# Kernel tuning notes

Hardware: AMD Instinct MI355X
Metric: run time of the kernel (lower is better)

Reference implementation:

```python
import jax, jax.numpy as jnp
import numpy as np

B, N, F_IN = 32, 512, 64
HEADS = (8, 8)
HIDS = (64, 64)
EDGE_P = 0.05  # graph density
NEG_SLOPE = 0.2
NEG_INF = -1e20


def setup_inputs() -> dict:
    key = jax.random.key(0)
    ks = jax.random.split(key, 8)
    x = jax.random.normal(ks[0], (B, N, F_IN), dtype=jnp.float32)
    adj = (jax.random.uniform(ks[1], (B, N, N)) < EDGE_P).astype(jnp.float32)
    adj = jnp.maximum(adj, adj.transpose(0, 2, 1))  # symmetric adjacency
    # mask = (batch, row): every (b, n) pair gets the masked softmax
    b_idx = jnp.repeat(jnp.arange(B, dtype=jnp.int32), N)   # [B*N]
    r_idx = jnp.tile(jnp.arange(N, dtype=jnp.int32), B)     # [B*N]
    # layer 0: f_in=64 -> f_out=64, H=8 ; layer 1: f_in=64*8=512 -> f_out=64, H=8
    W0 = jax.random.normal(ks[2], (F_IN, HIDS[0]), dtype=jnp.float32) / jnp.sqrt(jnp.float32(F_IN))
    a_src0 = jax.random.normal(ks[3], (HIDS[0], HEADS[0]), dtype=jnp.float32) / jnp.sqrt(jnp.float32(HIDS[0]))
    a_dst0 = jax.random.normal(ks[4], (HIDS[0], HEADS[0]), dtype=jnp.float32) / jnp.sqrt(jnp.float32(HIDS[0]))
    f_in1 = HIDS[0] * HEADS[0]
    W1 = jax.random.normal(ks[5], (f_in1, HIDS[1]), dtype=jnp.float32) / jnp.sqrt(jnp.float32(f_in1))
    a_src1 = jax.random.normal(ks[6], (HIDS[1], HEADS[1]), dtype=jnp.float32) / jnp.sqrt(jnp.float32(HIDS[1]))
    a_dst1 = jax.random.normal(ks[7], (HIDS[1], HEADS[1]), dtype=jnp.float32) / jnp.sqrt(jnp.float32(HIDS[1]))
    return dict(x=x, adj=adj, b_idx=b_idx, r_idx=r_idx,
                W0=W0, a_src0=a_src0, a_dst0=a_dst0,
                W1=W1, a_src1=a_src1, a_dst1=a_dst1)


def _gat_layer(x, adj, b_idx, r_idx, W, a_src, a_dst):
    # x: [B,N,f_in], adj: [B,N,N] (diag already set), W: [f_in,F], a_*: [F,H]
    hp = x @ W                                        # [B,N,F]
    s = jnp.einsum('bnf,fh->bhn', hp, a_src)          # attn_src
    d = jnp.einsum('bnf,fh->bhn', hp, a_dst)          # attn_dst
    attn = s[:, :, :, None] + d[:, :, None, :]        # [B,H,N,N]
    attn = jnp.where(attn >= 0, attn, NEG_SLOPE * attn)  # leaky_relu(0.2)
    attn = jnp.where(adj[:, None, :, :] == 0, 0.0, attn)  # masked_fill(adj==0, 0)
    rows = attn[b_idx, :, r_idx, :]                   # [K,H,N]
    rows = jnp.where(rows == 0.0, NEG_INF, rows)
    rows = jax.nn.softmax(rows, axis=-1)
    attn = attn.at[b_idx, :, r_idx, :].set(rows)
    return jnp.einsum('bhij,bjf->bhif', attn, hp)     # [B,H,N,F]


def reference(x, adj, b_idx, r_idx, W0, a_src0, a_dst0, W1, a_src1, a_dst1):
    Bn, Nn = x.shape[:2]
    # torch mutates adj in place: adj[batch,row,row] = 1 (self loops)
    adj = adj.at[b_idx, r_idx, r_idx].set(1.0)
    o = _gat_layer(x, adj, b_idx, r_idx, W0, a_src0, a_dst0)      # [B,H,N,F0]
    x1 = jax.nn.elu(o.transpose(0, 2, 1, 3).reshape(Bn, Nn, -1))  # [B,N,H*F0]
    o2 = _gat_layer(x1, adj, b_idx, r_idx, W1, a_src1, a_dst1)    # [B,H,N,F1]
    return o2.mean(axis=1)                                        # [B,N,F1]
```

## Files before the change

kernel.cpp:

```cpp
#include <hip/hip_runtime.h>
#include <hip/hip_bf16.h>
#include <math.h>

#define BB 32
#define NN 512

typedef _Float16 f16x8 __attribute__((ext_vector_type(8)));
typedef __fp16  fp16x2 __attribute__((ext_vector_type(2)));
typedef float f32x4 __attribute__((ext_vector_type(4)));

#define MFMA16(a, b, c) __builtin_amdgcn_mfma_f32_16x16x32_f16(a, b, c, 0, 0, 0)

union AF { f16x8 v; unsigned int u[4]; };

__device__ __forceinline__ void gload_lds16(const void* g, void* l) {
    __builtin_amdgcn_global_load_lds(
        (const __attribute__((address_space(1))) unsigned int*)g,
        (__attribute__((address_space(3))) unsigned int*)l, 16, 0, 0);
}

__global__ __launch_bounds__(256) void k_wt_prep(
    const float* __restrict__ W0, _Float16* __restrict__ W0T,
    const float* __restrict__ W1, _Float16* __restrict__ W1T)
{
    int id = blockIdx.x * 256 + threadIdx.x;
    const float* W; _Float16* WT; int KT, task;
    if (id < 512) { W = W0; WT = W0T; KT = 64;  task = id; }
    else          { W = W1; WT = W1T; KT = 512; task = id - 512; }
    int n = task & 63, gabs = task >> 6;
    int c = gabs >> 3, g = gabs & 7;
    f16x8 hv;
#pragma unroll
    for (int e = 0; e < 8; ++e)
        hv[e] = (_Float16)W[(size_t)(gabs * 8 + e) * 64 + n];
    *(f16x8*)(WT + (size_t)n * KT + c * 64 + (g ^ (n & 7)) * 8) = hv;
}

__global__ __launch_bounds__(256) void k_maxd(
    const float* __restrict__ dTg, float* __restrict__ maxd)
{
    __shared__ float sm[4];
    int bh = blockIdx.x;
    int t = threadIdx.x, lane = t & 63, w = t >> 6;
    const float* p = dTg + (size_t)bh * NN;
    float m = fmaxf(p[t], p[t + 256]);
#pragma unroll
    for (int off = 32; off; off >>= 1) m = fmaxf(m, __shfl_xor(m, off));
    if (lane == 0) sm[w] = m;
    __syncthreads();
    if (t == 0) maxd[bh] = fmaxf(fmaxf(sm[0], sm[1]), fmaxf(sm[2], sm[3]));
}

static __device__ __forceinline__ void epi_sd_hpt(
    const float* ctile, const float* asd_f, int row0, int t,
    float* __restrict__ s, float* __restrict__ dTg, _Float16* __restrict__ hpT)
{
    int b = row0 >> 9, jb = row0 & 511;
    if (t < 128) {
        int rr = t >> 3, h = t & 7;
        float sv = 0.f, dv = 0.f;
#pragma unroll
        for (int f = 0; f < 64; ++f) {
            float hv = ctile[rr * 66 + f];
            sv = fmaf(hv, asd_f[f * 8 + h], sv);
            dv = fmaf(hv, asd_f[512 + f * 8 + h], dv);
        }
        s[((size_t)b * NN + jb + rr) * 8 + h] = sv;
        dTg[((size_t)b * 8 + h) * NN + jb + rr] = dv;
    } else {
        int t2 = t - 128;
        int f = t2 >> 1, jl = (t2 & 1) * 8;
        f16x8 hv;
#pragma unroll
        for (int e = 0; e < 8; ++e)
            hv[e] = (_Float16)ctile[(jl + e) * 66 + f];
        *(f16x8*)(hpT + ((size_t)b * 64 + f) * NN + jb + jl) = hv;
    }
}

__global__ __launch_bounds__(256) void k_gemm0(
    const float* __restrict__ x, const _Float16* __restrict__ W0T,
    const float* __restrict__ a_src, const float* __restrict__ a_dst,
    const float* __restrict__ adj, unsigned long long* __restrict__ adjb,
    float* __restrict__ s, float* __restrict__ dTg, _Float16* __restrict__ hpT)
{
    __shared__ float ctile[16 * 66];
    __shared__ float asd_f[1024];
    __shared__ unsigned int mrow[16][16];
    int t = threadIdx.x, row0 = blockIdx.x * 16;
    int lane = t & 63, w = t >> 6, cn = lane & 15, rq = lane >> 4;

    int ar = t >> 4, seg = t & 15;
    const float* ap = adj + (size_t)(row0 + ar) * NN + seg * 32;
    float4 av[8];
#pragma unroll
    for (int q = 0; q < 8; ++q) av[q] = ((const float4*)ap)[q];

    ((float4*)asd_f)[t] = (t < 128) ? ((const float4*)a_src)[t]
                                    : ((const float4*)a_dst)[t - 128];
    f32x4 acc;
#pragma unroll
    for (int e = 0; e < 4; ++e) acc[e] = 0.f;
#pragma unroll
    for (int ks = 0; ks < 2; ++ks) {
        const float* xp = x + (size_t)(row0 + cn) * 64 + ks * 32 + rq * 8;
        float4 x0 = *(const float4*)xp, x1 = *(const float4*)(xp + 4);
        f16x8 ah = {(_Float16)x0.x, (_Float16)x0.y, (_Float16)x0.z, (_Float16)x0.w,
                    (_Float16)x1.x, (_Float16)x1.y, (_Float16)x1.z, (_Float16)x1.w};
        int nn = w * 16 + cn;
        f16x8 bh = *(const f16x8*)(W0T + (size_t)nn * 64 + (((ks * 4 + rq) ^ (nn & 7)) * 8));
        acc = MFMA16(ah, bh, acc);
    }
#pragma unroll
    for (int r = 0; r < 4; ++r)
        ctile[(rq * 4 + r) * 66 + w * 16 + cn] = acc[r];
    __syncthreads();
    epi_sd_hpt(ctile, asd_f, row0, t, s, dTg, hpT);

    unsigned int m32 = 0;
#pragma unroll
    for (int q = 0; q < 8; ++q) {
        if (av[q].x != 0.f) m32 |= 1u << (q * 4 + 0);
        if (av[q].y != 0.f) m32 |= 1u << (q * 4 + 1);
        if (av[q].z != 0.f) m32 |= 1u << (q * 4 + 2);
        if (av[q].w != 0.f) m32 |= 1u << (q * 4 + 3);
    }
    int i = (row0 + ar) & (NN - 1);
    if ((i >> 5) == seg) m32 |= 1u << (i & 31);
    mrow[ar][seg] = m32;
    __syncthreads();
    if (t < 128) {
        int r = t >> 3, k = t & 7;
        unsigned long long u = (unsigned long long)mrow[r][2 * k]
                             | ((unsigned long long)mrow[r][2 * k + 1] << 32);
        adjb[(size_t)(row0 + r) * 8 + k] = u;
    }
}

#define LD8(DST0, DST1, J)                                              \
    do {                                                                \
        *(float4*)&DST0[0] = *(const float4*)(dg0 + (J));               \
        *(float4*)&DST0[4] = *(const float4*)(dg0 + (J) + 4);           \
        *(float4*)&DST1[0] = *(const float4*)(dg1 + (J));               \
        *(float4*)&DST1[4] = *(const float4*)(dg1 + (J) + 4);           \
    } while (0)

#define PSTEP(DD0v, DD1v, MBYTE, KS, HTC)                               \
    do {                                                                \
        AF aA, aB;                                                      \
        _Pragma("unroll")                                               \
        for (int e = 0; e < 8; e += 2) {                                \
            float pA[2], pB[2];                                         \
            _Pragma("unroll")                                           \
            for (int q = 0; q < 2; ++q) {                               \
                int ee = e + q;                                         \
                bool con = (MBYTE >> ee) & 1u;                          \
                float e0 = sv0 + DD0v[ee];                              \
                float l0 = fmaxf(e0, 0.2f * e0);                        \
                float p0 = __expf(l0 - M0);                             \
                pA[q] = (con && l0 != 0.f) ? p0 : 0.f;                  \
                float e1 = sv1 + DD1v[ee];                              \
                float l1 = fmaxf(e1, 0.2f * e1);                        \
                float p1 = __expf(l1 - M1);                             \
                pB[q] = (con && l1 != 0.f) ? p1 : 0.f;                  \
            }                                                           \
            fp16x2 ka = __builtin_amdgcn_cvt_pkrtz(pA[0], pA[1]);       \
            fp16x2 kb = __builtin_amdgcn_cvt_pkrtz(pB[0], pB[1]);       \
            aA.u[e >> 1] = __builtin_bit_cast(unsigned int, ka);        \
            aB.u[e >> 1] = __builtin_bit_cast(unsigned int, kb);        \
        }                                                               \
        accrs[0] = MFMA16(aA.v, ones, accrs[0]);                        \
        accrs[1] = MFMA16(aB.v, ones, accrs[1]);                        \
        _Pragma("unroll")                                               \
        for (int ft = 0; ft < 4; ++ft) {                                \
            int f = ft * 16 + cn;                                       \
            f16x8 bh = *(const f16x8*)&HTC[f * 64 + ((((KS) * 4 + rq) ^ (f & 7)) * 8)]; \
            acc[0][ft] = MFMA16(aA.v, bh, acc[0][ft]);                  \
            acc[1][ft] = MFMA16(aB.v, bh, acc[1][ft]);                  \
        }                                                               \
    } while (0)

template<int MODE>
__global__ __launch_bounds__(256, 4) void k_attn_fused(
    const unsigned long long* __restrict__ adjb, const float* __restrict__ s,
    const float* __restrict__ dTg, const float* __restrict__ maxd,
    const _Float16* __restrict__ hpT,
    const _Float16* __restrict__ W1T,
    const float* __restrict__ a_src, const float* __restrict__ a_dst,
    float* __restrict__ s_out, float* __restrict__ dTg_out,
    _Float16* __restrict__ hpT_out, float* __restrict__ o_f)
{
    __shared__ __align__(16) char smem[32768];
    _Float16* hTd0 = (_Float16*)smem;
    _Float16* hTd1 = (_Float16*)(smem + 8192);

    int blk = blockIdx.x;
    int vb = ((blk & 7) << 7) | (blk >> 3);
    int b = vb >> 5, i0 = (vb & 31) << 4;
    int row0 = vb * 16;
    int t = threadIdx.x, lane = t & 63, w = t >> 6;
    int cn = lane & 15, rq = lane >> 4;
    int h0 = 2 * w, h1 = h0 + 1;
    int myrow = i0 + cn;

    const _Float16* hb = hpT + (size_t)b * 64 * NN;

    int f0 = t >> 3, g0 = t & 7;
    const _Float16* src0 = hb + (size_t)f0 * NN + ((g0 ^ (f0 & 7)) * 8);
    const _Float16* src1 = hb + (size_t)(f0 + 32) * NN + ((g0 ^ (f0 & 7)) * 8);
    {
        _Float16* db = hTd0 + (w << 9);
        gload_lds16(src0, db);
        gload_lds16(src1, db + 2048);
    }

    float sv0 = s[((size_t)b * NN + myrow) * 8 + h0];
    float sv1 = s[((size_t)b * NN + myrow) * 8 + h1];
    float M0 = fmaxf(sv0 + maxd[b * 8 + h0], 0.f);
    float M1 = fmaxf(sv1 + maxd[b * 8 + h1], 0.f);

    const float* dg0 = dTg + ((size_t)b * 8 + h0) * NN;
    const float* dg1 = dTg + ((size_t)b * 8 + h1) * NN;
    const unsigned long long* abr = adjb + ((size_t)b * NN + myrow) * 8;
    int rq8 = rq * 8;

    f16x8 ones;
#pragma unroll
    for (int e = 0; e < 8; ++e) ones[e] = (_Float16)1.0f;

    f32x4 acc[2][4], accrs[2];
#pragma unroll
    for (int hh = 0; hh < 2; ++hh) {
#pragma unroll
        for (int e = 0; e < 4; ++e) accrs[hh][e] = 0.f;
#pragma unroll
        for (int ft = 0; ft < 4; ++ft)
#pragma unroll
            for (int e = 0; e < 4; ++e) acc[hh][ft][e] = 0.f;
    }

    float ddA0[8], ddA1[8], ddB0[8], ddB1[8];
    unsigned long long mb = abr[0];
    LD8(ddA0, ddA1, rq8);
    __syncthreads();

    for (int jcx = 0; jcx < 8; ++jcx) {
        int jc = jcx * 64;
        const _Float16* hTc = (jcx & 1) ? hTd1 : hTd0;
        if (jcx < 7) {
            _Float16* db = ((jcx & 1) ? hTd0 : hTd1) + (w << 9);
            gload_lds16(src0 + jc + 64, db);
            gload_lds16(src1 + jc + 64, db + 2048);
        }
        unsigned long long mbn = (jcx < 7) ? abr[jcx + 1] : 0ull;
        unsigned int ml = (unsigned int)mb, mhh = (unsigned int)(mb >> 32);
        LD8(ddB0, ddB1, jc + 32 + rq8);
        {
            unsigned int mby = (ml >> rq8) & 0xffu;
            PSTEP(ddA0, ddA1, mby, 0, hTc);
        }
        if (jcx < 7) LD8(ddA0, ddA1, jc + 64 + rq8);
        {
            unsigned int mby = (mhh >> rq8) & 0xffu;
            PSTEP(ddB0, ddB1, mby, 1, hTc);
        }
        mb = mbn;
        __syncthreads();
    }

    float invr[2][4];
#pragma unroll
    for (int hh = 0; hh < 2; ++hh)
#pragma unroll
        for (int r = 0; r < 4; ++r) invr[hh][r] = 1.0f / accrs[hh][r];

    if (MODE == 0) {
        _Float16* Bst0 = (_Float16*)smem;
        _Float16* Bst1 = (_Float16*)(smem + 8192);
        const _Float16* wsrc = W1T + (size_t)(t >> 3) * 512 + ((t & 7) * 8);
        {
            _Float16* db = Bst0 + (w << 9);
            gload_lds16(wsrc, db);
            gload_lds16(wsrc + 32 * 512, db + 2048);
        }
        _Float16* x1all = (_Float16*)(smem + 16384);
#pragma unroll
        for (int hh = 0; hh < 2; ++hh) {
            int h = h0 + hh;
#pragma unroll
            for (int ft = 0; ft < 4; ++ft)
#pragma unroll
                for (int r = 0; r < 4; ++r) {
                    int il = rq * 4 + r;
                    float v = acc[hh][ft][r] * invr[hh][r];
                    v = v > 0.f ? v : __expf(v) - 1.f;
                    int f = ft * 16 + cn;
                    x1all[h * 1024 + il * 64 + (((f >> 3) ^ (il & 7)) * 8) + (f & 7)] =
                        (_Float16)v;
                }
        }
        __syncthreads();
        f32x4 g1;
#pragma unroll
        for (int e = 0; e < 4; ++e) g1[e] = 0.f;
        for (int kc = 0; kc < 8; ++kc) {
            const _Float16* Bc = (kc & 1) ? Bst1 : Bst0;
            if (kc < 7) {
                _Float16* db = ((kc & 1) ? Bst0 : Bst1) + (w << 9);
                gload_lds16(wsrc + (kc + 1) * 64, db);
                gload_lds16(wsrc + 32 * 512 + (kc + 1) * 64, db + 2048);
            }
#pragma unroll
            for (int ks = 0; ks < 2; ++ks) {
                int pa = (((ks * 4 + rq) ^ (cn & 7)) * 8);
                f16x8 ah = *(const f16x8*)&x1all[kc * 1024 + cn * 64 + pa];
                int nn = w * 16 + cn;
                f16x8 bh = *(const f16x8*)&Bc[nn * 64 + (((ks * 4 + rq) ^ (nn & 7)) * 8)];
                g1 = MFMA16(ah, bh, g1);
            }
            __syncthreads();
        }
        float* ctile = (float*)(smem + 16384);
        float* asd_f = (float*)(smem + 24576);
#pragma unroll
        for (int r = 0; r < 4; ++r)
            ctile[(rq * 4 + r) * 66 + w * 16 + cn] = g1[r];
        ((float4*)asd_f)[t] = (t < 128) ? ((const float4*)a_src)[t]
                                        : ((const float4*)a_dst)[t - 128];
        __syncthreads();
        epi_sd_hpt(ctile, asd_f, row0, t, s_out, dTg_out, hpT_out);
    } else {
        float* red = (float*)smem;
#pragma unroll
        for (int ft = 0; ft < 4; ++ft)
#pragma unroll
            for (int r = 0; r < 4; ++r) {
                int il = rq * 4 + r;
                float v = acc[0][ft][r] * invr[0][r]
                        + acc[1][ft][r] * invr[1][r];
                red[(w * 16 + il) * 64 + ft * 16 + cn] = v;
            }
        __syncthreads();
#pragma unroll
        for (int u = 0; u < 4; ++u) {
            int idx = t + u * 256;
            int il = idx >> 6, f = idx & 63;
            float sum = red[il * 64 + f] + red[(16 + il) * 64 + f]
                      + red[(32 + il) * 64 + f] + red[(48 + il) * 64 + f];
            o_f[((size_t)b * NN + i0 + il) * 64 + f] = sum * 0.125f;
        }
    }
}

extern "C" void kernel_launch(void* const* d_in, const int* in_sizes, int n_in,
                              void* d_out, int out_size, void* d_ws, size_t ws_size,
                              hipStream_t stream) {
    const float* x      = (const float*)d_in[0];
    const float* adj    = (const float*)d_in[1];
    const float* W0     = (const float*)d_in[4];
    const float* a_src0 = (const float*)d_in[5];
    const float* a_dst0 = (const float*)d_in[6];
    const float* W1     = (const float*)d_in[7];
    const float* a_src1 = (const float*)d_in[8];
    const float* a_dst1 = (const float*)d_in[9];
    float* out = (float*)d_out;

    float* ws = (float*)d_ws;
    const size_t R = (size_t)BB * NN;
    const size_t BHN = (size_t)BB * 8 * NN;
    float* s0    = ws;
    float* dTg0  = s0 + R * 8;
    float* s1    = dTg0 + BHN;
    float* dTg1  = s1 + R * 8;
    float* maxd0 = dTg1 + BHN;
    float* maxd1 = maxd0 + 256;
    _Float16* hp0T = (_Float16*)(maxd1 + 256);
    _Float16* hp1T = hp0T + (size_t)BB * 64 * NN;
    _Float16* W0T  = hp1T + (size_t)BB * 64 * NN;
    _Float16* W1T  = W0T + (size_t)64 * 64;
    unsigned long long* adjb = (unsigned long long*)(W1T + (size_t)64 * 512);

    k_wt_prep<<<18, 256, 0, stream>>>(W0, W0T, W1, W1T);
    k_gemm0<<<1024, 256, 0, stream>>>(x, W0T, a_src0, a_dst0, adj, adjb,
                                      s0, dTg0, hp0T);
    k_maxd<<<256, 256, 0, stream>>>(dTg0, maxd0);
    k_attn_fused<0><<<1024, 256, 0, stream>>>(adjb, s0, dTg0, maxd0, hp0T,
                                              W1T, a_src1, a_dst1,
                                              s1, dTg1, hp1T, nullptr);
    k_maxd<<<256, 256, 0, stream>>>(dTg1, maxd1);
    k_attn_fused<1><<<1024, 256, 0, stream>>>(adjb, s1, dTg1, maxd1, hp1T,
                                              nullptr, nullptr, nullptr,
                                              nullptr, nullptr, nullptr, out);
}
```

Before: 159.7 us.

## Stage dst scores through LDS in 128-column chunks; read W1T directly

```diff
diff --git a/kernel.cpp b/kernel.cpp
--- a/kernel.cpp
+++ b/kernel.cpp
@@ -136,14 +136,6 @@
         adjb[(size_t)(row0 + r) * 8 + k] = u;
     }
 }
-
-#define LD8(DST0, DST1, J)                                              \
-    do {                                                                \
-        *(float4*)&DST0[0] = *(const float4*)(dg0 + (J));               \
-        *(float4*)&DST0[4] = *(const float4*)(dg0 + (J) + 4);           \
-        *(float4*)&DST1[0] = *(const float4*)(dg1 + (J));               \
-        *(float4*)&DST1[4] = *(const float4*)(dg1 + (J) + 4);           \
-    } while (0)
 
 #define PSTEP(DD0v, DD1v, MBYTE, KS, HTC)                               \
     do {                                                                \
@@ -180,6 +172,17 @@
         }                                                               \
     } while (0)
 
+#define STAGE_SC(SC, B)                                                  \
+    do {                                                                 \
+        _Float16* t0_ = (_Float16*)(B) + (w << 9);                       \
+        _Float16* t1_ = (_Float16*)((B) + 8192) + (w << 9);              \
+        gload_lds16(src0 + (SC) * 128, t0_);                             \
+        gload_lds16(src1 + (SC) * 128, t0_ + 2048);                      \
+        gload_lds16(src0 + (SC) * 128 + 64, t1_);                        \
+        gload_lds16(src1 + (SC) * 128 + 64, t1_ + 2048);                 \
+        gload_lds16(dsrc + (SC) * 128, (float*)((B) + 16384) + (w << 8));\
+    } while (0)
+
 template<int MODE>
 __global__ __launch_bounds__(256, 4) void k_attn_fused(
     const unsigned long long* __restrict__ adjb, const float* __restrict__ s,
@@ -190,9 +193,7 @@
     float* __restrict__ s_out, float* __restrict__ dTg_out,
     _Float16* __restrict__ hpT_out, float* __restrict__ o_f)
 {
-    __shared__ __align__(16) char smem[32768];
-    _Float16* hTd0 = (_Float16*)smem;
-    _Float16* hTd1 = (_Float16*)(smem + 8192);
+    __shared__ __align__(16) char smem[40960];
 
     int blk = blockIdx.x;
     int vb = ((blk & 7) << 7) | (blk >> 3);
@@ -204,25 +205,25 @@
     int myrow = i0 + cn;
 
     const _Float16* hb = hpT + (size_t)b * 64 * NN;
-
     int f0 = t >> 3, g0 = t & 7;
     const _Float16* src0 = hb + (size_t)f0 * NN + ((g0 ^ (f0 & 7)) * 8);
     const _Float16* src1 = hb + (size_t)(f0 + 32) * NN + ((g0 ^ (f0 & 7)) * 8);
-    {
-        _Float16* db = hTd0 + (w << 9);
-        gload_lds16(src0, db);
-        gload_lds16(src1, db + 2048);
-    }
+    const float* dgB = dTg + (size_t)b * 8 * NN;
+    int hs = h0 + (lane >> 5), js = (lane & 31) * 4;
+    const float* dsrc = dgB + (size_t)hs * NN + js;
+
+    char* bufP = smem;
+    char* bufQ = smem + 20480;
+
+    STAGE_SC(0, bufP);
 
     float sv0 = s[((size_t)b * NN + myrow) * 8 + h0];
     float sv1 = s[((size_t)b * NN + myrow) * 8 + h1];
     float M0 = fmaxf(sv0 + maxd[b * 8 + h0], 0.f);
     float M1 = fmaxf(sv1 + maxd[b * 8 + h1], 0.f);
-
-    const float* dg0 = dTg + ((size_t)b * 8 + h0) * NN;
-    const float* dg1 = dTg + ((size_t)b * 8 + h1) * NN;
     const unsigned long long* abr = adjb + ((size_t)b * NN + myrow) * 8;
     int rq8 = rq * 8;
+    unsigned long long mb0 = abr[0], mb1 = abr[1];
 
     f16x8 ones;
 #pragma unroll
@@ -239,32 +240,34 @@
             for (int e = 0; e < 4; ++e) acc[hh][ft][e] = 0.f;
     }
 
-    float ddA0[8], ddA1[8], ddB0[8], ddB1[8];
-    unsigned long long mb = abr[0];
-    LD8(ddA0, ddA1, rq8);
     __syncthreads();
 
-    for (int jcx = 0; jcx < 8; ++jcx) {
-        int jc = jcx * 64;
-        const _Float16* hTc = (jcx & 1) ? hTd1 : hTd0;
-        if (jcx < 7) {
-            _Float16* db = ((jcx & 1) ? hTd0 : hTd1) + (w << 9);
-            gload_lds16(src0 + jc + 64, db);
-            gload_lds16(src1 + jc + 64, db + 2048);
-        }
-        unsigned long long mbn = (jcx < 7) ? abr[jcx + 1] : 0ull;
-        unsigned int ml = (unsigned int)mb, mhh = (unsigned int)(mb >> 32);
-        LD8(ddB0, ddB1, jc + 32 + rq8);
-        {
-            unsigned int mby = (ml >> rq8) & 0xffu;
-            PSTEP(ddA0, ddA1, mby, 0, hTc);
-        }
-        if (jcx < 7) LD8(ddA0, ddA1, jc + 64 + rq8);
-        {
-            unsigned int mby = (mhh >> rq8) & 0xffu;
-            PSTEP(ddB0, ddB1, mby, 1, hTc);
-        }
-        mb = mbn;
+    for (int sc = 0; sc < 4; ++sc) {
+        char* cur = (sc & 1) ? bufQ : bufP;
+        char* nxt = (sc & 1) ? bufP : bufQ;
+        if (sc < 3) STAGE_SC(sc + 1, nxt);
+        unsigned long long nm0 = 0, nm1 = 0;
+        if (sc < 3) { nm0 = abr[2 * sc + 2]; nm1 = abr[2 * sc + 3]; }
+        const float* ddl0 = (const float*)(cur + 16384) + h0 * 128;
+        const float* ddl1 = ddl0 + 128;
+#pragma unroll
+        for (int half = 0; half < 2; ++half) {
+            unsigned long long mbc = half ? mb1 : mb0;
+            unsigned int ml = (unsigned int)mbc, mh = (unsigned int)(mbc >> 32);
+            const _Float16* hTc = (const _Float16*)(cur + half * 8192);
+#pragma unroll
+            for (int ks = 0; ks < 2; ++ks) {
+                int jrel = half * 64 + ks * 32 + rq8;
+                unsigned int mby = ((ks ? mh : ml) >> rq8) & 0xffu;
+                float dd0[8], dd1[8];
+                *(float4*)&dd0[0] = *(const float4*)(ddl0 + jrel);
+                *(float4*)&dd0[4] = *(const float4*)(ddl0 + jrel + 4);
+                *(float4*)&dd1[0] = *(const float4*)(ddl1 + jrel);
+                *(float4*)&dd1[4] = *(const float4*)(ddl1 + jrel + 4);
+                PSTEP(dd0, dd1, mby, ks, hTc);
+            }
+        }
+        mb0 = nm0; mb1 = nm1;
         __syncthreads();
     }
 
@@ -275,14 +278,6 @@
         for (int r = 0; r < 4; ++r) invr[hh][r] = 1.0f / accrs[hh][r];
 
     if (MODE == 0) {
-        _Float16* Bst0 = (_Float16*)smem;
-        _Float16* Bst1 = (_Float16*)(smem + 8192);
-        const _Float16* wsrc = W1T + (size_t)(t >> 3) * 512 + ((t & 7) * 8);
-        {
-            _Float16* db = Bst0 + (w << 9);
-            gload_lds16(wsrc, db);
-            gload_lds16(wsrc + 32 * 512, db + 2048);
-        }
         _Float16* x1all = (_Float16*)(smem + 16384);
 #pragma unroll
         for (int hh = 0; hh < 2; ++hh) {
@@ -303,23 +298,20 @@
         f32x4 g1;
 #pragma unroll
         for (int e = 0; e < 4; ++e) g1[e] = 0.f;
+        int nn = w * 16 + cn;
+        const _Float16* wb = W1T + (size_t)nn * 512;
+#pragma unroll
         for (int kc = 0; kc < 8; ++kc) {
-            const _Float16* Bc = (kc & 1) ? Bst1 : Bst0;
-            if (kc < 7) {
-                _Float16* db = ((kc & 1) ? Bst0 : Bst1) + (w << 9);
-                gload_lds16(wsrc + (kc + 1) * 64, db);
-                gload_lds16(wsrc + 32 * 512 + (kc + 1) * 64, db + 2048);
-            }
 #pragma unroll
             for (int ks = 0; ks < 2; ++ks) {
-                int pa = (((ks * 4 + rq) ^ (cn & 7)) * 8);
-                f16x8 ah = *(const f16x8*)&x1all[kc * 1024 + cn * 64 + pa];
-                int nn = w * 16 + cn;
-                f16x8 bh = *(const f16x8*)&Bc[nn * 64 + (((ks * 4 + rq) ^ (nn & 7)) * 8)];
+                f16x8 ah = *(const f16x8*)&x1all[kc * 1024 + cn * 64 +
+                                                 (((ks * 4 + rq) ^ (cn & 7)) * 8)];
+                f16x8 bh = *(const f16x8*)(wb + kc * 64 +
+                                           (((ks * 4 + rq) ^ (nn & 7)) * 8));
                 g1 = MFMA16(ah, bh, g1);
             }
-            __syncthreads();
-        }
+        }
+        __syncthreads();
         float* ctile = (float*)(smem + 16384);
         float* asd_f = (float*)(smem + 24576);
 #pragma unroll
```

Result: no change. 156.9 us (-1.7%).
